# Optimization experiments

Hardware: AMD Instinct MI355X
Metric: run time of the kernel (lower is better)

Reference implementation:

```python
import jax, jax.numpy as jnp
import numpy as np

N_TREES, N_LEAVES, PATH_LEN, N_NODES, D, B = 10, 16, 5, 31, 256, 4096


def _local_paths():
    # root-to-leaf paths of a full binary tree, depth 4: 31 nodes, 16 leaves, path len 5
    return np.array([[0, 1 + l // 8, 3 + l // 4, 7 + l // 2, 15 + l]
                     for l in range(N_LEAVES)], np.int32)


def setup_inputs() -> dict:
    key = jax.random.key(0)
    k1, k2, k3, k4, k5, k6 = jax.random.split(key, 6)
    # one activated leaf per tree -> multi-hot cross_features (B, N_TREES*N_LEAVES)
    leaf = jax.random.randint(k1, (B, N_TREES), 0, N_LEAVES)
    cross = jnp.zeros((B, N_TREES, N_LEAVES), jnp.float32)
    cross = cross.at[jnp.arange(B)[:, None], jnp.arange(N_TREES)[None, :], leaf].set(1.0)
    cross_features = cross.reshape(B, N_TREES * N_LEAVES)
    # learned params: node embedding table + single-layer LSTM (torch init scale 1/sqrt(D))
    emb = jax.random.normal(k2, (N_TREES * N_NODES, D), jnp.float32) * 0.02
    s = 1.0 / np.sqrt(D)
    W_ih = jax.random.uniform(k3, (4 * D, D), jnp.float32, -s, s)
    W_hh = jax.random.uniform(k4, (4 * D, D), jnp.float32, -s, s)
    b_ih = jax.random.uniform(k5, (4 * D,), jnp.float32, -s, s)
    b_hh = jax.random.uniform(k6, (4 * D,), jnp.float32, -s, s)
    return {"cross_features": cross_features, "emb": emb, "W_ih": W_ih,
            "W_hh": W_hh, "b_ih": b_ih, "b_hh": b_hh}


def reference(cross_features, emb, W_ih, W_hh, b_ih, b_hh):
    # global path node ids per (tree, leaf): [T, L, P]
    gpaths = jnp.asarray(_local_paths())[None, :, :] + \
        (jnp.arange(N_TREES, dtype=jnp.int32) * N_NODES)[:, None, None]
    # activated leaf per tree (exactly one hot per 16-leaf block)
    leaf = jnp.argmax(cross_features.reshape(B, N_TREES, N_LEAVES), axis=-1)  # [B, T]
    node_ids = gpaths[jnp.arange(N_TREES)[None, :], leaf]                     # [B, T, P]
    x = emb[node_ids].reshape(B * N_TREES, PATH_LEN, D)                       # packed paths
    # precompute input projections for all steps: [N, P, 4D]
    xg = jnp.einsum('npd,gd->npg', x, W_ih) + (b_ih + b_hh)

    def step(carry, xt):
        h, c = carry
        g = xt + h @ W_hh.T
        i, f, gg, o = jnp.split(g, 4, axis=-1)  # torch gate order: i, f, g, o
        c = jax.nn.sigmoid(f) * c + jax.nn.sigmoid(i) * jnp.tanh(gg)
        h = jax.nn.sigmoid(o) * jnp.tanh(c)
        return (h, c), None

    n = B * N_TREES
    h0 = jnp.zeros((n, D), x.dtype)
    (h, _), _ = jax.lax.scan(step, (h0, h0), jnp.swapaxes(xg, 0, 1))
    return h.reshape(B, N_TREES, D)
```

## Files before the change

kernel.cpp:

```cpp
#include <hip/hip_runtime.h>

#define NT 10
#define NL 16
#define NN 31
#define DD 256
#define G4 1024
#define NNODES (NT*NN)
#define NPATH (NT*NL)
#define NB 4096

__device__ __forceinline__ float sigf(float x)   { return 1.0f / (1.0f + __expf(-x)); }
__device__ __forceinline__ float tanh_f(float x) { return 2.0f / (1.0f + __expf(-2.0f*x)) - 1.0f; }

__global__ __launch_bounds__(256) void k_nodeproj(
    const float* __restrict__ emb, const float* __restrict__ Wih,
    const float* __restrict__ bih, const float* __restrict__ bhh,
    float* __restrict__ xg)
{
    __shared__ float smem[20 * 260 + 20 * 4 * 64];
    float4* es4 = (float4*)smem;
    float*  ps  = smem + 20 * 260;

    const int tid = threadIdx.x;
    const int nt  = blockIdx.x & 15;
    const int mt  = blockIdx.x >> 4;
    const int kq  = tid >> 6;
    const int w   = tid & 63;

    const float4* W4 = (const float4*)Wih + (size_t)(nt * 64 + w) * 64 + kq * 16;
    float4 wr[16];
    #pragma unroll
    for (int j = 0; j < 16; ++j) wr[j] = W4[j];

    const float4* emb4 = (const float4*)emb;
    #pragma unroll
    for (int r = 0; r < 5; ++r) {
        int idx = tid + 256 * r;
        int m = idx >> 6, q = idx & 63;
        int n = mt * 20 + m;
        es4[m * 65 + q] = (n < NNODES) ? emb4[(size_t)n * 64 + q]
                                       : make_float4(0.f, 0.f, 0.f, 0.f);
    }
    __syncthreads();

    float acc[20];
    #pragma unroll
    for (int m = 0; m < 20; ++m) acc[m] = 0.f;
    #pragma unroll
    for (int j = 0; j < 16; ++j) {
        float4 wv = wr[j];
        #pragma unroll
        for (int m = 0; m < 20; ++m) {
            float4 h = es4[m * 65 + kq * 16 + j];
            acc[m] = fmaf(wv.x, h.x, fmaf(wv.y, h.y,
                     fmaf(wv.z, h.z, fmaf(wv.w, h.w, acc[m]))));
        }
    }
    #pragma unroll
    for (int m = 0; m < 20; ++m) ps[(m * 4 + kq) * 64 + w] = acc[m];
    __syncthreads();

    const int nl   = tid & 63;
    const int msub = tid >> 6;
    const int j    = nt * 64 + nl;
    const float bsum = bih[j] + bhh[j];
    #pragma unroll
    for (int r = 0; r < 5; ++r) {
        int m = msub * 5 + r;
        int n = mt * 20 + m;
        float s = ps[(m * 4 + 0) * 64 + nl] + ps[(m * 4 + 1) * 64 + nl]
                + ps[(m * 4 + 2) * 64 + nl] + ps[(m * 4 + 3) * 64 + nl];
        if (n < NNODES) xg[(size_t)n * G4 + j] = s + bsum;
    }
}

template<int S>
__global__ __launch_bounds__(256) void k_step(
    const float* __restrict__ xg, const float* __restrict__ Whh,
    const float* __restrict__ hprev, const float* __restrict__ cprev,
    float* __restrict__ hout, float* __restrict__ cout)
{
    constexpr int L = 1 << (S - 1);
    __shared__ float hs [L * DD];
    __shared__ float ps [L * DD];
    __shared__ float csl[L * 16];

    const int tid  = threadIdx.x;
    const int t    = blockIdx.x >> 4;
    const int dt   = blockIdx.x & 15;
    const int kq   = tid >> 6;
    const int w    = tid & 63;
    const int gate = w >> 4;
    const int col  = w & 15;

    const float4* W4 = (const float4*)Whh
        + (size_t)(gate * DD + dt * 16 + col) * 64 + kq * 16;
    float4 wreg[16];
    #pragma unroll
    for (int j = 0; j < 16; ++j) wreg[j] = W4[j];

    if constexpr (S == 1) {
        const float* xr = xg + (size_t)(t * NN) * G4;
        float xi = xr[tid], xgg = xr[512 + tid], xo = xr[768 + tid];
        float c0 = sigf(xi) * tanh_f(xgg);
        float h0 = sigf(xo) * tanh_f(c0);
        hs[tid] = h0;
        if ((tid >> 4) == dt) csl[tid & 15] = c0;
    } else {
        #pragma unroll
        for (int rr = 0; rr < L; ++rr)
            hs[rr * DD + tid] = hprev[(size_t)(t * L + rr) * DD + tid];
        if (tid < L * 16)
            csl[tid] = cprev[(size_t)(t * L + (tid >> 4)) * DD
                             + dt * 16 + (tid & 15)];
    }
    __syncthreads();

    const float4* hs4 = (const float4*)hs;
    float acc[L];
    #pragma unroll
    for (int p = 0; p < L; ++p) acc[p] = 0.f;
    #pragma unroll
    for (int j = 0; j < 16; ++j) {
        float4 wv = wreg[j];
        #pragma unroll
        for (int p = 0; p < L; ++p) {
            float4 h = hs4[p * 64 + kq * 16 + j];
            acc[p] = fmaf(wv.x, h.x, fmaf(wv.y, h.y,
                     fmaf(wv.z, h.z, fmaf(wv.w, h.w, acc[p]))));
        }
    }
    #pragma unroll
    for (int p = 0; p < L; ++p) ps[p * DD + kq * 64 + w] = acc[p];
    __syncthreads();

    if (tid < 32 * L) {
        const int p    = tid >> 5;
        const int ch   = (tid >> 4) & 1;
        const int c2   = tid & 15;
        const int q    = p * 2 + ch;
        const int node = ((1 << S) - 1) + q;
        const float* xn = xg + (size_t)(t * NN + node) * G4 + dt * 16 + c2;

        float g0 = 0.f, g1 = 0.f, g2 = 0.f, g3 = 0.f;
        #pragma unroll
        for (int k = 0; k < 4; ++k) {
            const float* pp = ps + p * DD + k * 64;
            g0 += pp[ 0 + c2]; g1 += pp[16 + c2];
            g2 += pp[32 + c2]; g3 += pp[48 + c2];
        }
        float gi = g0 + xn[0];
        float gf = g1 + xn[256];
        float gg = g2 + xn[512];
        float go = g3 + xn[768];
        float cin = csl[p * 16 + c2];
        float cn  = sigf(gf) * cin + sigf(gi) * tanh_f(gg);
        float hn  = sigf(go) * tanh_f(cn);

        size_t orow = (size_t)(t * 2 * L + q);
        hout[orow * DD + dt * 16 + c2] = hn;
        if constexpr (S < 4) cout[orow * DD + dt * 16 + c2] = cn;
    }
}

__global__ __launch_bounds__(256) void k_scatter(
    const float* __restrict__ cross, const float* __restrict__ htab,
    float* __restrict__ out)
{
    const int tid  = threadIdx.x;
    const int wave = tid >> 6;
    const int lane = tid & 63;
    const int r = blockIdx.x * 4 + wave;
    const int b = r / NT;
    const int t = r - b * NT;

    float v = 0.f;
    if (lane < NL) v = cross[(size_t)b * (NT * NL) + t * NL + lane];
    unsigned long long m = __ballot(v > 0.5f);
    int leaf = m ? (int)__builtin_ctzll(m) : 0;
    int p = t * NL + leaf;

    const float4* h4 = (const float4*)htab;
    float4* o4 = (float4*)out;
    o4[(size_t)r * 64 + lane] = h4[(size_t)p * 64 + lane];
}

extern "C" void kernel_launch(void* const* d_in, const int* in_sizes, int n_in,
                              void* d_out, int out_size, void* d_ws, size_t ws_size,
                              hipStream_t stream)
{
    const float* cross = (const float*)d_in[0];
    const float* emb   = (const float*)d_in[1];
    const float* Wih   = (const float*)d_in[2];
    const float* Whh   = (const float*)d_in[3];
    const float* bih   = (const float*)d_in[4];
    const float* bhh   = (const float*)d_in[5];
    float* out = (float*)d_out;

    float* ws = (float*)d_ws;
    float* xg = ws;
    float* h1 = xg + (size_t)NNODES * G4;
    float* c1 = h1 + 20 * DD;
    float* h2 = c1 + 20 * DD;
    float* c2 = h2 + 40 * DD;
    float* h3 = c2 + 40 * DD;
    float* c3 = h3 + 80 * DD;
    float* h4 = c3 + 80 * DD;

    hipLaunchKernelGGL(k_nodeproj, dim3(256), dim3(256), 0, stream,
                       emb, Wih, bih, bhh, xg);
    hipLaunchKernelGGL(HIP_KERNEL_NAME(k_step<1>), dim3(160), dim3(256), 0, stream,
                       xg, Whh, (const float*)nullptr, (const float*)nullptr, h1, c1);
    hipLaunchKernelGGL(HIP_KERNEL_NAME(k_step<2>), dim3(160), dim3(256), 0, stream,
                       xg, Whh, h1, c1, h2, c2);
    hipLaunchKernelGGL(HIP_KERNEL_NAME(k_step<3>), dim3(160), dim3(256), 0, stream,
                       xg, Whh, h2, c2, h3, c3);
    hipLaunchKernelGGL(HIP_KERNEL_NAME(k_step<4>), dim3(160), dim3(256), 0, stream,
                       xg, Whh, h3, c3, h4, (float*)nullptr);
    hipLaunchKernelGGL(k_scatter, dim3(10240), dim3(256), 0, stream,
                       cross, h4, out);
}
```

Measured before the change: 117.4 us.

## Fuse four LSTM tree-step kernels into one persistent kernel with per-tree flags

Replaces the four per-level step launches with a single kernel. Blocks of the same tree synchronise through global atomic counters: each of the 16 column blocks bumps a per-tree flag after writing its h slice, and the others spin-wait until 16 more arrivals are seen. The c state stays in shared memory, since each block owns its own column slice, and the xg inputs for all levels are prefetched into registers up front. This is meant to remove three launch gaps and the c round-trips through global memory, at the cost of spin-wait latency and relying on all 160 blocks being co-resident.

```diff
diff --git a/kernel.cpp b/kernel.cpp
--- a/kernel.cpp
+++ b/kernel.cpp
@@ -9,8 +9,15 @@
 #define NPATH (NT*NL)
 #define NB 4096
 
+__device__ unsigned g_tf[3][NT][32];
+
 __device__ __forceinline__ float sigf(float x)   { return 1.0f / (1.0f + __expf(-x)); }
 __device__ __forceinline__ float tanh_f(float x) { return 2.0f / (1.0f + __expf(-2.0f*x)) - 1.0f; }
+
+__device__ __forceinline__ void co_store(float* p, float v) {
+    union { float f; unsigned u; } c; c.f = v;
+    __hip_atomic_store((unsigned*)p, c.u, __ATOMIC_RELAXED, __HIP_MEMORY_SCOPE_AGENT);
+}
 
 __global__ __launch_bounds__(256) void k_nodeproj(
     const float* __restrict__ emb, const float* __restrict__ Wih,
@@ -74,16 +81,14 @@
     }
 }
 
-template<int S>
-__global__ __launch_bounds__(256) void k_step(
+__global__ __launch_bounds__(256) void k_treesteps(
     const float* __restrict__ xg, const float* __restrict__ Whh,
-    const float* __restrict__ hprev, const float* __restrict__ cprev,
-    float* __restrict__ hout, float* __restrict__ cout)
-{
-    constexpr int L = 1 << (S - 1);
-    __shared__ float hs [L * DD];
-    __shared__ float ps [L * DD];
-    __shared__ float csl[L * 16];
+    float* __restrict__ h1g, float* __restrict__ h2g,
+    float* __restrict__ h3g, float* __restrict__ h4g)
+{
+    __shared__ float hs[8 * DD];
+    __shared__ float ps[8 * DD];
+    __shared__ float cbuf[2][8 * 16];
 
     const int tid  = threadIdx.x;
     const int t    = blockIdx.x >> 4;
@@ -93,73 +98,122 @@
     const int gate = w >> 4;
     const int col  = w & 15;
 
+    const unsigned base = __hip_atomic_load(&g_tf[2][t][0],
+        __ATOMIC_RELAXED, __HIP_MEMORY_SCOPE_AGENT);
+
     const float4* W4 = (const float4*)Whh
         + (size_t)(gate * DD + dt * 16 + col) * 64 + kq * 16;
     float4 wreg[16];
     #pragma unroll
     for (int j = 0; j < 16; ++j) wreg[j] = W4[j];
 
-    if constexpr (S == 1) {
+    float xnv[4][4];
+    #pragma unroll
+    for (int s = 1; s <= 4; ++s) {
+        xnv[s-1][0] = 0.f; xnv[s-1][1] = 0.f;
+        xnv[s-1][2] = 0.f; xnv[s-1][3] = 0.f;
+        if (tid < (32 << (s - 1))) {
+            int node = (1 << s) - 1 + (tid >> 4);
+            const float* xn = xg + (size_t)(t * NN + node) * G4 + dt * 16 + (tid & 15);
+            xnv[s-1][0] = xn[0];
+            xnv[s-1][1] = xn[256];
+            xnv[s-1][2] = xn[512];
+            xnv[s-1][3] = xn[768];
+        }
+    }
+
+    {
         const float* xr = xg + (size_t)(t * NN) * G4;
-        float xi = xr[tid], xgg = xr[512 + tid], xo = xr[768 + tid];
-        float c0 = sigf(xi) * tanh_f(xgg);
-        float h0 = sigf(xo) * tanh_f(c0);
+        float r_i = xr[tid], r_g = xr[512 + tid], r_o = xr[768 + tid];
+        float c0 = sigf(r_i) * tanh_f(r_g);
+        float h0 = sigf(r_o) * tanh_f(c0);
         hs[tid] = h0;
-        if ((tid >> 4) == dt) csl[tid & 15] = c0;
-    } else {
-        #pragma unroll
-        for (int rr = 0; rr < L; ++rr)
-            hs[rr * DD + tid] = hprev[(size_t)(t * L + rr) * DD + tid];
-        if (tid < L * 16)
-            csl[tid] = cprev[(size_t)(t * L + (tid >> 4)) * DD
-                             + dt * 16 + (tid & 15)];
+        if ((tid >> 4) == dt) cbuf[0][tid & 15] = c0;
     }
     __syncthreads();
 
-    const float4* hs4 = (const float4*)hs;
-    float acc[L];
-    #pragma unroll
-    for (int p = 0; p < L; ++p) acc[p] = 0.f;
-    #pragma unroll
-    for (int j = 0; j < 16; ++j) {
-        float4 wv = wreg[j];
-        #pragma unroll
-        for (int p = 0; p < L; ++p) {
-            float4 h = hs4[p * 64 + kq * 16 + j];
-            acc[p] = fmaf(wv.x, h.x, fmaf(wv.y, h.y,
-                     fmaf(wv.z, h.z, fmaf(wv.w, h.w, acc[p]))));
-        }
-    }
-    #pragma unroll
-    for (int p = 0; p < L; ++p) ps[p * DD + kq * 64 + w] = acc[p];
-    __syncthreads();
-
-    if (tid < 32 * L) {
-        const int p    = tid >> 5;
-        const int ch   = (tid >> 4) & 1;
-        const int c2   = tid & 15;
-        const int q    = p * 2 + ch;
-        const int node = ((1 << S) - 1) + q;
-        const float* xn = xg + (size_t)(t * NN + node) * G4 + dt * 16 + c2;
-
-        float g0 = 0.f, g1 = 0.f, g2 = 0.f, g3 = 0.f;
-        #pragma unroll
-        for (int k = 0; k < 4; ++k) {
-            const float* pp = ps + p * DD + k * 64;
-            g0 += pp[ 0 + c2]; g1 += pp[16 + c2];
-            g2 += pp[32 + c2]; g3 += pp[48 + c2];
-        }
-        float gi = g0 + xn[0];
-        float gf = g1 + xn[256];
-        float gg = g2 + xn[512];
-        float go = g3 + xn[768];
-        float cin = csl[p * 16 + c2];
-        float cn  = sigf(gf) * cin + sigf(gi) * tanh_f(gg);
-        float hn  = sigf(go) * tanh_f(cn);
-
-        size_t orow = (size_t)(t * 2 * L + q);
-        hout[orow * DD + dt * 16 + c2] = hn;
-        if constexpr (S < 4) cout[orow * DD + dt * 16 + c2] = cn;
+    float* hout[3] = { h1g, h2g, h3g };
+    const float* hin[3] = { h1g, h2g, h3g };
+
+    #pragma unroll
+    for (int s = 1; s <= 4; ++s) {
+        const int L = 1 << (s - 1);
+
+        if (s > 1) {
+            if (tid < 64) {
+                const unsigned tgt = base + 16u;
+                while (__hip_atomic_load(&g_tf[s - 2][t][0],
+                        __ATOMIC_RELAXED, __HIP_MEMORY_SCOPE_AGENT) < tgt)
+                    __builtin_amdgcn_s_sleep(2);
+            }
+            __syncthreads();
+            const unsigned long long* src =
+                (const unsigned long long*)(hin[s - 2] + (size_t)t * L * DD);
+            unsigned long long raw[4];
+            #pragma unroll
+            for (int r = 0; r < L / 2; ++r)
+                raw[r] = __hip_atomic_load(src + tid + 256 * r,
+                    __ATOMIC_RELAXED, __HIP_MEMORY_SCOPE_AGENT);
+            float2* hs2 = (float2*)hs;
+            #pragma unroll
+            for (int r = 0; r < L / 2; ++r) {
+                union { unsigned long long u; float2 f; } cv; cv.u = raw[r];
+                hs2[tid + 256 * r] = cv.f;
+            }
+            __syncthreads();
+        }
+
+        const float4* hs4 = (const float4*)hs;
+        float acc[8];
+        #pragma unroll
+        for (int p = 0; p < 8; ++p) acc[p] = 0.f;
+        #pragma unroll
+        for (int j = 0; j < 16; ++j) {
+            float4 wv = wreg[j];
+            #pragma unroll
+            for (int p = 0; p < L; ++p) {
+                float4 h = hs4[p * 64 + kq * 16 + j];
+                acc[p] = fmaf(wv.x, h.x, fmaf(wv.y, h.y,
+                         fmaf(wv.z, h.z, fmaf(wv.w, h.w, acc[p]))));
+            }
+        }
+        #pragma unroll
+        for (int p = 0; p < L; ++p) ps[p * DD + kq * 64 + w] = acc[p];
+        __syncthreads();
+
+        if (tid < 32 * L) {
+            const int p  = tid >> 5;
+            const int c2 = tid & 15;
+            const int q  = tid >> 4;
+            float g0 = 0.f, g1 = 0.f, g2 = 0.f, g3 = 0.f;
+            #pragma unroll
+            for (int k = 0; k < 4; ++k) {
+                const float* pp = ps + p * DD + k * 64;
+                g0 += pp[ 0 + c2]; g1 += pp[16 + c2];
+                g2 += pp[32 + c2]; g3 += pp[48 + c2];
+            }
+            float gi = g0 + xnv[s - 1][0];
+            float gf = g1 + xnv[s - 1][1];
+            float gg = g2 + xnv[s - 1][2];
+            float go = g3 + xnv[s - 1][3];
+            float cin = cbuf[(s - 1) & 1][p * 16 + c2];
+            float cn  = sigf(gf) * cin + sigf(gi) * tanh_f(gg);
+            float hn  = sigf(go) * tanh_f(cn);
+            if (s < 4) {
+                cbuf[s & 1][q * 16 + c2] = cn;
+                co_store(hout[s - 1] + (size_t)(t * 2 * L + q) * DD
+                                     + dt * 16 + c2, hn);
+            } else {
+                h4g[(size_t)(t * NL + q) * DD + dt * 16 + c2] = hn;
+            }
+        }
+
+        if (s < 4) {
+            __syncthreads();
+            if (tid == 0)
+                __hip_atomic_fetch_add(&g_tf[s - 1][t][0], 1u,
+                    __ATOMIC_RELAXED, __HIP_MEMORY_SCOPE_AGENT);
+        }
     }
 }
 
@@ -200,23 +254,14 @@
     float* ws = (float*)d_ws;
     float* xg = ws;
     float* h1 = xg + (size_t)NNODES * G4;
-    float* c1 = h1 + 20 * DD;
-    float* h2 = c1 + 20 * DD;
-    float* c2 = h2 + 40 * DD;
-    float* h3 = c2 + 40 * DD;
-    float* c3 = h3 + 80 * DD;
-    float* h4 = c3 + 80 * DD;
+    float* h2 = h1 + 20 * DD;
+    float* h3 = h2 + 40 * DD;
+    float* h4 = h3 + 80 * DD;
 
     hipLaunchKernelGGL(k_nodeproj, dim3(256), dim3(256), 0, stream,
                        emb, Wih, bih, bhh, xg);
-    hipLaunchKernelGGL(HIP_KERNEL_NAME(k_step<1>), dim3(160), dim3(256), 0, stream,
-                       xg, Whh, (const float*)nullptr, (const float*)nullptr, h1, c1);
-    hipLaunchKernelGGL(HIP_KERNEL_NAME(k_step<2>), dim3(160), dim3(256), 0, stream,
-                       xg, Whh, h1, c1, h2, c2);
-    hipLaunchKernelGGL(HIP_KERNEL_NAME(k_step<3>), dim3(160), dim3(256), 0, stream,
-                       xg, Whh, h2, c2, h3, c3);
-    hipLaunchKernelGGL(HIP_KERNEL_NAME(k_step<4>), dim3(160), dim3(256), 0, stream,
-                       xg, Whh, h3, c3, h4, (float*)nullptr);
+    hipLaunchKernelGGL(k_treesteps, dim3(160), dim3(256), 0, stream,
+                       xg, Whh, h1, h2, h3, h4);
     hipLaunchKernelGGL(k_scatter, dim3(10240), dim3(256), 0, stream,
                        cross, h4, out);
 }
```

Result: faster. 111.8 us (-4.8%).

## Fuse four LSTM step kernels into one persistent per-tree kernel

Applied to the files above, without the earlier changes.

Replaces the four per-level step launches with a single kernel that runs one 1024-thread block per tree. Each thread keeps a slice of all four gate rows of W_hh in registers, and h/c state is double-buffered in shared memory across tree levels. This removes the inter-kernel launches and the global round trips for h and c. In exchange, only 10 workgroups run, each must stream the whole W_hh. Holding 256 floats of weights per thread at 1024 threads per block will likely cause heavy register spilling.

```diff
diff --git a/kernel.cpp b/kernel.cpp
--- a/kernel.cpp
+++ b/kernel.cpp
@@ -6,7 +6,6 @@
 #define DD 256
 #define G4 1024
 #define NNODES (NT*NN)
-#define NPATH (NT*NL)
 #define NB 4096
 
 __device__ __forceinline__ float sigf(float x)   { return 1.0f / (1.0f + __expf(-x)); }
@@ -74,92 +73,95 @@
     }
 }
 
-template<int S>
-__global__ __launch_bounds__(256) void k_step(
+__global__ __launch_bounds__(1024, 1) void k_monolstm(
     const float* __restrict__ xg, const float* __restrict__ Whh,
-    const float* __restrict__ hprev, const float* __restrict__ cprev,
-    float* __restrict__ hout, float* __restrict__ cout)
-{
-    constexpr int L = 1 << (S - 1);
-    __shared__ float hs [L * DD];
-    __shared__ float ps [L * DD];
-    __shared__ float csl[L * 16];
-
-    const int tid  = threadIdx.x;
-    const int t    = blockIdx.x >> 4;
-    const int dt   = blockIdx.x & 15;
-    const int kq   = tid >> 6;
-    const int w    = tid & 63;
-    const int gate = w >> 4;
-    const int col  = w & 15;
-
-    const float4* W4 = (const float4*)Whh
-        + (size_t)(gate * DD + dt * 16 + col) * 64 + kq * 16;
-    float4 wreg[16];
-    #pragma unroll
-    for (int j = 0; j < 16; ++j) wreg[j] = W4[j];
-
-    if constexpr (S == 1) {
-        const float* xr = xg + (size_t)(t * NN) * G4;
-        float xi = xr[tid], xgg = xr[512 + tid], xo = xr[768 + tid];
+    float* __restrict__ h4g)
+{
+    __shared__ float hsA[8 * DD], hsB[8 * DD];
+    __shared__ float clA[8 * DD], clB[8 * DD];
+
+    const int tid = threadIdx.x;
+    const int t   = blockIdx.x;
+    const int d   = tid >> 2;
+    const int q   = tid & 3;
+
+    const float4* W4 = (const float4*)Whh;
+    float4 w0[16], w1[16], w2[16], w3[16];
+    #pragma unroll
+    for (int j = 0; j < 16; ++j) {
+        w0[j] = W4[(size_t)(          d) * 64 + q * 16 + j];
+        w1[j] = W4[(size_t)(256     + d) * 64 + q * 16 + j];
+        w2[j] = W4[(size_t)(512     + d) * 64 + q * 16 + j];
+        w3[j] = W4[(size_t)(768     + d) * 64 + q * 16 + j];
+    }
+
+    const float* xr = xg + (size_t)t * NN * G4;
+    if (q == 0) {
+        float xi  = xr[d];
+        float xgg = xr[512 + d];
+        float xo  = xr[768 + d];
         float c0 = sigf(xi) * tanh_f(xgg);
-        float h0 = sigf(xo) * tanh_f(c0);
-        hs[tid] = h0;
-        if ((tid >> 4) == dt) csl[tid & 15] = c0;
-    } else {
-        #pragma unroll
-        for (int rr = 0; rr < L; ++rr)
-            hs[rr * DD + tid] = hprev[(size_t)(t * L + rr) * DD + tid];
-        if (tid < L * 16)
-            csl[tid] = cprev[(size_t)(t * L + (tid >> 4)) * DD
-                             + dt * 16 + (tid & 15)];
+        hsA[d] = sigf(xo) * tanh_f(c0);
+        clA[d] = c0;
     }
     __syncthreads();
 
-    const float4* hs4 = (const float4*)hs;
-    float acc[L];
-    #pragma unroll
-    for (int p = 0; p < L; ++p) acc[p] = 0.f;
-    #pragma unroll
-    for (int j = 0; j < 16; ++j) {
-        float4 wv = wreg[j];
+    float* hsP = hsA; float* hsC = hsB;
+    float* clP = clA; float* clC = clB;
+
+    #pragma unroll
+    for (int s = 1; s <= 4; ++s) {
+        const int L = 1 << (s - 1);
+
         #pragma unroll
         for (int p = 0; p < L; ++p) {
-            float4 h = hs4[p * 64 + kq * 16 + j];
-            acc[p] = fmaf(wv.x, h.x, fmaf(wv.y, h.y,
-                     fmaf(wv.z, h.z, fmaf(wv.w, h.w, acc[p]))));
+            const float4* hp = (const float4*)(hsP + p * DD) + q * 16;
+            float4 a0 = make_float4(0.f, 0.f, 0.f, 0.f);
+            float4 a1 = a0, a2 = a0, a3 = a0;
+            #pragma unroll
+            for (int j = 0; j < 16; ++j) {
+                float4 hv = hp[j];
+                a0.x = fmaf(w0[j].x, hv.x, a0.x); a0.y = fmaf(w0[j].y, hv.y, a0.y);
+                a0.z = fmaf(w0[j].z, hv.z, a0.z); a0.w = fmaf(w0[j].w, hv.w, a0.w);
+                a1.x = fmaf(w1[j].x, hv.x, a1.x); a1.y = fmaf(w1[j].y, hv.y, a1.y);
+                a1.z = fmaf(w1[j].z, hv.z, a1.z); a1.w = fmaf(w1[j].w, hv.w, a1.w);
+                a2.x = fmaf(w2[j].x, hv.x, a2.x); a2.y = fmaf(w2[j].y, hv.y, a2.y);
+                a2.z = fmaf(w2[j].z, hv.z, a2.z); a2.w = fmaf(w2[j].w, hv.w, a2.w);
+                a3.x = fmaf(w3[j].x, hv.x, a3.x); a3.y = fmaf(w3[j].y, hv.y, a3.y);
+                a3.z = fmaf(w3[j].z, hv.z, a3.z); a3.w = fmaf(w3[j].w, hv.w, a3.w);
+            }
+            float g0 = (a0.x + a0.y) + (a0.z + a0.w);
+            float g1 = (a1.x + a1.y) + (a1.z + a1.w);
+            float g2 = (a2.x + a2.y) + (a2.z + a2.w);
+            float g3 = (a3.x + a3.y) + (a3.z + a3.w);
+            g0 += __shfl_xor(g0, 1); g0 += __shfl_xor(g0, 2);
+            g1 += __shfl_xor(g1, 1); g1 += __shfl_xor(g1, 2);
+            g2 += __shfl_xor(g2, 1); g2 += __shfl_xor(g2, 2);
+            g3 += __shfl_xor(g3, 1); g3 += __shfl_xor(g3, 2);
+
+            if (q < 2) {
+                const int child = 2 * p + q;
+                const int node  = (1 << s) - 1 + child;
+                const float* xn = xg + ((size_t)t * NN + node) * G4;
+                float gi = g0 + xn[      d];
+                float gf = g1 + xn[256 + d];
+                float gg = g2 + xn[512 + d];
+                float go = g3 + xn[768 + d];
+                float cin = clP[p * DD + d];
+                float cn  = sigf(gf) * cin + sigf(gi) * tanh_f(gg);
+                float hn  = sigf(go) * tanh_f(cn);
+                if (s < 4) {
+                    hsC[child * DD + d] = hn;
+                    clC[child * DD + d] = cn;
+                } else {
+                    h4g[((size_t)t * NL + child) * DD + d] = hn;
+                }
+            }
         }
-    }
-    #pragma unroll
-    for (int p = 0; p < L; ++p) ps[p * DD + kq * 64 + w] = acc[p];
-    __syncthreads();
-
-    if (tid < 32 * L) {
-        const int p    = tid >> 5;
-        const int ch   = (tid >> 4) & 1;
-        const int c2   = tid & 15;
-        const int q    = p * 2 + ch;
-        const int node = ((1 << S) - 1) + q;
-        const float* xn = xg + (size_t)(t * NN + node) * G4 + dt * 16 + c2;
-
-        float g0 = 0.f, g1 = 0.f, g2 = 0.f, g3 = 0.f;
-        #pragma unroll
-        for (int k = 0; k < 4; ++k) {
-            const float* pp = ps + p * DD + k * 64;
-            g0 += pp[ 0 + c2]; g1 += pp[16 + c2];
-            g2 += pp[32 + c2]; g3 += pp[48 + c2];
-        }
-        float gi = g0 + xn[0];
-        float gf = g1 + xn[256];
-        float gg = g2 + xn[512];
-        float go = g3 + xn[768];
-        float cin = csl[p * 16 + c2];
-        float cn  = sigf(gf) * cin + sigf(gi) * tanh_f(gg);
-        float hn  = sigf(go) * tanh_f(cn);
-
-        size_t orow = (size_t)(t * 2 * L + q);
-        hout[orow * DD + dt * 16 + c2] = hn;
-        if constexpr (S < 4) cout[orow * DD + dt * 16 + c2] = cn;
+        __syncthreads();
+        float* tp;
+        tp = hsP; hsP = hsC; hsC = tp;
+        tp = clP; clP = clC; clC = tp;
     }
 }
 
@@ -197,26 +199,14 @@
     const float* bhh   = (const float*)d_in[5];
     float* out = (float*)d_out;
 
-    float* ws = (float*)d_ws;
-    float* xg = ws;
-    float* h1 = xg + (size_t)NNODES * G4;
-    float* c1 = h1 + 20 * DD;
-    float* h2 = c1 + 20 * DD;
-    float* c2 = h2 + 40 * DD;
-    float* h3 = c2 + 40 * DD;
-    float* c3 = h3 + 80 * DD;
-    float* h4 = c3 + 80 * DD;
+    float* ws  = (float*)d_ws;
+    float* xg  = ws;
+    float* h4g = xg + (size_t)NNODES * G4;
 
     hipLaunchKernelGGL(k_nodeproj, dim3(256), dim3(256), 0, stream,
                        emb, Wih, bih, bhh, xg);
-    hipLaunchKernelGGL(HIP_KERNEL_NAME(k_step<1>), dim3(160), dim3(256), 0, stream,
-                       xg, Whh, (const float*)nullptr, (const float*)nullptr, h1, c1);
-    hipLaunchKernelGGL(HIP_KERNEL_NAME(k_step<2>), dim3(160), dim3(256), 0, stream,
-                       xg, Whh, h1, c1, h2, c2);
-    hipLaunchKernelGGL(HIP_KERNEL_NAME(k_step<3>), dim3(160), dim3(256), 0, stream,
-                       xg, Whh, h2, c2, h3, c3);
-    hipLaunchKernelGGL(HIP_KERNEL_NAME(k_step<4>), dim3(160), dim3(256), 0, stream,
-                       xg, Whh, h3, c3, h4, (float*)nullptr);
+    hipLaunchKernelGGL(k_monolstm, dim3(NT), dim3(1024), 0, stream,
+                       xg, Whh, h4g);
     hipLaunchKernelGGL(k_scatter, dim3(10240), dim3(256), 0, stream,
-                       cross, h4, out);
-}
+                       cross, h4g, out);
+}
```

New measurement: 441.3 us. 276% more time.
